# Kernel tuning notes

Measured on AMD Instinct MI355X. Metric: run time of the kernel, lower is better.

The kernel has to match this reference:

```python
import jax, jax.numpy as jnp
import numpy as np

DIM = 768
HEADS = 12
N_PATCH = 1024
ORDER = 5
DECAY = 0.5
EPS = 1e-6


def _exact_mask(N, order, decay):
    # 2D grid graph adjacency, row-major node order (matches sorted nx.grid_2d_graph nodes)
    side = int(np.sqrt(N))
    A = np.zeros((N, N), dtype=np.float64)
    idx = np.arange(N)
    r, c = idx // side, idx % side
    right = idx[c < side - 1]
    A[right, right + 1] = 1.0
    A[right + 1, right] = 1.0
    down = idx[r < side - 1]
    A[down, down + side] = 1.0
    A[down + side, down] = 1.0
    D_inv = 1.0 / np.maximum(A.sum(axis=1), 1.0)
    W = D_inv[:, None] * A
    M = np.eye(N)
    W_k = np.eye(N)
    coeff = 1.0
    for _ in range(order):
        W_k = W_k @ W
        coeff *= decay
        M += coeff * W_k
    M = M / M.sum(axis=1, keepdims=True)
    return jnp.asarray(M, dtype=jnp.float32)


def setup_inputs() -> dict:
    key = jax.random.key(0)
    k1, k2, k3, k4 = jax.random.split(key, 4)
    B = 4
    x = jax.random.normal(k1, (B, N_PATCH, DIM), dtype=jnp.float32)
    # nn.Linear(dim, 3*dim, bias=False): store as [dim, 3*dim] for x @ W
    scale = 1.0 / np.sqrt(DIM)
    W_qkv = jax.random.uniform(k2, (DIM, 3 * DIM), dtype=jnp.float32, minval=-scale, maxval=scale)
    W_out = jax.random.uniform(k3, (DIM, DIM), dtype=jnp.float32, minval=-scale, maxval=scale)
    b_out = jax.random.uniform(k4, (DIM,), dtype=jnp.float32, minval=-scale, maxval=scale)
    mask = _exact_mask(N_PATCH, ORDER, DECAY)
    return {"x": x, "W_qkv": W_qkv, "W_out": W_out, "b_out": b_out, "mask": mask}


def reference(x, W_qkv, W_out, b_out, mask):
    B, N, C = x.shape
    H, D = HEADS, C // HEADS
    qkv = x @ W_qkv  # [B, N, 3C]
    q, k, v = jnp.split(qkv, 3, axis=-1)
    # [B, N, C] -> [B, H, N, D]
    q, k, v = (t.reshape(B, N, H, D).transpose(0, 2, 1, 3) for t in (q, k, v))
    # feature map
    q = jax.nn.relu(q) + EPS
    k = jax.nn.relu(k) + EPS
    # (q^T @ M)^T = M^T @ q  ->  einsum over node axis
    q_graph = jnp.einsum('nm,bhnd->bhmd', mask, q)
    k_graph = jnp.einsum('nm,bhnd->bhmd', mask, k)
    q = q + 0.1 * q_graph
    k = k + 0.1 * k_graph
    linear_kernel = jnp.einsum('bhnd,bhmd->bhnm', q, k)  # [B, H, N, N]
    masked_kernel = linear_kernel * mask[None, None, :, :]
    z = 1.0 / (masked_kernel.sum(axis=-1, keepdims=True) + EPS)  # [B, H, N, 1]
    out = jnp.einsum('bhnm,bhmd->bhnd', masked_kernel, v) * z
    out = out.transpose(0, 2, 1, 3).reshape(B, N, C)
    return out @ W_out + b_out
```

## Files before the change

### kernel.cpp

```cpp
#include <hip/hip_runtime.h>

#define NP   1024
#define DIM  768
#define NH   12
#define HD   64
#define TQ   2304
#define EPS  1e-6f

typedef __attribute__((ext_vector_type(8))) short bf16x8;
typedef __attribute__((ext_vector_type(4))) float f32x4;

#define MFMA(a, b, c) __builtin_amdgcn_mfma_f32_16x16x32_bf16((a), (b), (c), 0, 0, 0)

__device__ __forceinline__ unsigned short f2b(float x) {
    unsigned int u = __builtin_bit_cast(unsigned int, x);
    u = (u + 0x7fffu + ((u >> 16) & 1u)) >> 16;
    return (unsigned short)u;
}
__device__ __forceinline__ float b2f(unsigned short h) {
    unsigned int u = ((unsigned int)h) << 16;
    return __builtin_bit_cast(float, u);
}
__device__ __forceinline__ void gld16(const void* g, void* l) {
    __builtin_amdgcn_global_load_lds((const __attribute__((address_space(1))) unsigned int*)g,
                                     (__attribute__((address_space(3))) unsigned int*)l,
                                     16, 0, 0);
}

__global__ __launch_bounds__(256) void k_prep(const float* __restrict__ x,
                                              const float* __restrict__ W_qkv,
                                              const float* __restrict__ W_out,
                                              const float* __restrict__ mask,
                                              unsigned short* __restrict__ xb,
                                              unsigned short* __restrict__ WqkvT,
                                              unsigned short* __restrict__ WoutT,
                                              unsigned short* __restrict__ maskT) {
    __shared__ float buf[64][65];
    const int bx = blockIdx.x, t = threadIdx.x;
    if (bx < 1536) {
        const int i = bx * 256 + t;
        const float4* p = (const float4*)x + (size_t)i * 2;
        float4 a = p[0], b = p[1];
        alignas(16) unsigned short o[8] = {f2b(a.x), f2b(a.y), f2b(a.z), f2b(a.w),
                                           f2b(b.x), f2b(b.y), f2b(b.z), f2b(b.w)};
        *(uint4*)(xb + (size_t)i * 8) = *(const uint4*)o;
        return;
    }
    const float* in; unsigned short* outp; int R, C, ct, rt;
    if (bx < 1968)      { int q = bx - 1536; in = W_qkv; outp = WqkvT; R = 768;  C = 2304; ct = q % 36; rt = q / 36; }
    else if (bx < 2112) { int q = bx - 1968; in = W_out; outp = WoutT; R = 768;  C = 768;  ct = q % 12; rt = q / 12; }
    else                { int q = bx - 2112; in = mask;  outp = maskT; R = 1024; C = 1024; ct = q % 16; rt = q / 16; }
    const int r0 = rt * 64, c0 = ct * 64;
    const int rr = t >> 4, cc = (t & 15) * 4;
    #pragma unroll
    for (int p = 0; p < 4; ++p) {
        float4 v = *(const float4*)(in + (size_t)(r0 + p * 16 + rr) * C + c0 + cc);
        buf[p * 16 + rr][cc + 0] = v.x; buf[p * 16 + rr][cc + 1] = v.y;
        buf[p * 16 + rr][cc + 2] = v.z; buf[p * 16 + rr][cc + 3] = v.w;
    }
    __syncthreads();
    const int oc = t >> 2, orr = (t & 3) * 16;
    alignas(16) unsigned short tmp[16];
    #pragma unroll
    for (int j = 0; j < 16; ++j) tmp[j] = f2b(buf[orr + j][oc]);
    unsigned short* dst = outp + (size_t)(c0 + oc) * R + r0 + orr;
    *(uint4*)dst = *(const uint4*)tmp;
    *(uint4*)(dst + 8) = *(const uint4*)(tmp + 8);
}

__global__ __launch_bounds__(256) void k_gemm1(const unsigned short* __restrict__ A,
                                               const unsigned short* __restrict__ Bt,
                                               unsigned short* __restrict__ T) {
    __shared__ unsigned short As[128][32];
    __shared__ unsigned short Bs[128][32];
    const int tid = threadIdx.x, w = tid >> 6, l = tid & 63;
    const int m0 = blockIdx.y * 128, n0 = blockIdx.x * 128;
    const int wm = (w >> 1) * 64, wn = (w & 1) * 64;
    const int quad = l >> 4, col = l & 15;
    const int lr = l >> 2, lc = (l & 3) * 8;

    f32x4 acc[4][4] = {};
    for (int k0 = 0; k0 < DIM; k0 += 32) {
        gld16(A + (size_t)(m0 + w * 32 + lr) * DIM + k0 + lc, &As[w * 32][0]);
        gld16(A + (size_t)(m0 + w * 32 + 16 + lr) * DIM + k0 + lc, &As[w * 32 + 16][0]);
        gld16(Bt + (size_t)(n0 + w * 32 + lr) * DIM + k0 + lc, &Bs[w * 32][0]);
        gld16(Bt + (size_t)(n0 + w * 32 + 16 + lr) * DIM + k0 + lc, &Bs[w * 32 + 16][0]);
        __syncthreads();
        bf16x8 a[4], b[4];
        #pragma unroll
        for (int i = 0; i < 4; ++i) a[i] = *(const bf16x8*)&As[wm + i * 16 + col][quad * 8];
        #pragma unroll
        for (int j = 0; j < 4; ++j) b[j] = *(const bf16x8*)&Bs[wn + j * 16 + col][quad * 8];
        #pragma unroll
        for (int i = 0; i < 4; ++i)
            #pragma unroll
            for (int j = 0; j < 4; ++j)
                acc[i][j] = MFMA(a[i], b[j], acc[i][j]);
        __syncthreads();
    }

    const int cgb = n0 + wn;
    const int slot = cgb / DIM;
    const int h = (cgb % DIM) >> 6;
    const bool act = (slot < 2);
    const int sh = slot * 48 + (m0 >> 10) * NH + h;
    const int npb = (m0 & 1023) + wm + quad * 4;
    #pragma unroll
    for (int j = 0; j < 4; ++j) {
        unsigned short* dcol = T + ((size_t)(sh * HD + j * 16 + col)) * NP + npb;
        #pragma unroll
        for (int i = 0; i < 4; ++i) {
            alignas(8) unsigned short t4[4];
            #pragma unroll
            for (int r = 0; r < 4; ++r) {
                float v = acc[i][j][r];
                if (act) v = fmaxf(v, 0.f) + EPS;
                t4[r] = f2b(v);
            }
            *(uint2*)(dcol + i * 16) = *(const uint2*)t4;
        }
    }
}

__global__ __launch_bounds__(256) void k_graphmix(const unsigned short* __restrict__ maskT,
                                                  const unsigned short* __restrict__ T,
                                                  unsigned short* __restrict__ q2) {
    const int bh = blockIdx.y, mt = blockIdx.x;
    const int m0 = mt * 64, gr = 2 * mt;
    __shared__ unsigned short Ms[64][32], Fq[64][32], Fk[64][32];
    __shared__ unsigned short Sq[64][72], Sk[64][72];
    const int tid = threadIdx.x, w = tid >> 6, l = tid & 63;
    const int quad = l >> 4, col = l & 15;
    const int lr = l >> 2, lc = (l & 3) * 8;
    const unsigned short* Tq = T + (size_t)bh * HD * NP;
    const unsigned short* Tk = T + (size_t)(48 + bh) * HD * NP;

    f32x4 accq[4] = {}, acck[4] = {};
    const int r0 = max(0, gr - 5), r1 = min(31, gr + 6);
    for (int rw = r0; rw <= r1; ++rw) {
        const int nc = rw * 32;
        __syncthreads();
        gld16(maskT + (size_t)(m0 + w * 16 + lr) * NP + nc + lc, &Ms[w * 16][0]);
        gld16(Tq + (size_t)(w * 16 + lr) * NP + nc + lc, &Fq[w * 16][0]);
        gld16(Tk + (size_t)(w * 16 + lr) * NP + nc + lc, &Fk[w * 16][0]);
        __syncthreads();
        if (rw == gr || rw == gr + 1) {
            const int off = (rw - gr) * 32;
            *(uint4*)&Sq[w * 16 + lr][off + lc] = *(const uint4*)&Fq[w * 16 + lr][lc];
            *(uint4*)&Sk[w * 16 + lr][off + lc] = *(const uint4*)&Fk[w * 16 + lr][lc];
        }
        bf16x8 a = *(const bf16x8*)&Ms[w * 16 + col][quad * 8];
        #pragma unroll
        for (int dt = 0; dt < 4; ++dt) {
            accq[dt] = MFMA(a, *(const bf16x8*)&Fq[dt * 16 + col][quad * 8], accq[dt]);
            acck[dt] = MFMA(a, *(const bf16x8*)&Fk[dt * 16 + col][quad * 8], acck[dt]);
        }
    }
    __syncthreads();
    unsigned short* q2q = q2 + ((size_t)bh * NP + m0) * HD;
    unsigned short* q2k = q2 + ((size_t)(48 + bh) * NP + m0) * HD;
    #pragma unroll
    for (int dt = 0; dt < 4; ++dt)
        #pragma unroll
        for (int r = 0; r < 4; ++r) {
            const int ml = w * 16 + quad * 4 + r;
            const int d = dt * 16 + col;
            q2q[(size_t)ml * HD + d] = f2b(b2f(Sq[d][ml]) + 0.1f * accq[dt][r]);
            q2k[(size_t)ml * HD + d] = f2b(b2f(Sk[d][ml]) + 0.1f * acck[dt][r]);
        }
}

__global__ __launch_bounds__(256) void k_attn(const unsigned short* __restrict__ q2,
                                              const unsigned short* __restrict__ T,
                                              const float* __restrict__ mask,
                                              unsigned short* __restrict__ attnb) {
    const int bh = blockIdx.y, b = bh / NH, h = bh % NH;
    const int nt2 = blockIdx.x, n0 = nt2 * 128;
    __shared__ unsigned short Qs[2][128][32];
    __shared__ unsigned short Ks[2][64][32];
    __shared__ unsigned short VT[2][64][32];
    __shared__ unsigned short Ss[128][72];
    __shared__ float rowz[128];
    const int tid = threadIdx.x, w = tid >> 6, l = tid & 63;
    const int quad = l >> 4, col = l & 15;
    const int lr = l >> 2, lc = (l & 3) * 8;

    const unsigned short* qb = q2 + ((size_t)bh * NP + n0) * HD;
    const unsigned short* kb = q2 + (size_t)(48 + bh) * NP * HD;
    const unsigned short* vtb = T + (size_t)(96 + bh) * HD * NP;

    #pragma unroll
    for (int hh = 0; hh < 2; ++hh)
        #pragma unroll
        for (int c = 0; c < 2; ++c)
            gld16(qb + (size_t)(w * 32 + c * 16 + lr) * HD + hh * 32 + lc,
                  &Qs[hh][w * 32 + c * 16][0]);

    f32x4 oacc[2][4] = {};
    float racc[2][4] = {};
    const int mlo = max(0, 2 * nt2 - 3), mhi = min(15, 2 * nt2 + 4);

    for (int mt = mlo; mt <= mhi; ++mt) {
        const int m0 = mt * 64;
        float mreg[2][4][4];
        #pragma unroll
        for (int rg = 0; rg < 2; ++rg)
            #pragma unroll
            for (int mtt = 0; mtt < 4; ++mtt)
                #pragma unroll
                for (int r = 0; r < 4; ++r)
                    mreg[rg][mtt][r] = mask[(size_t)(n0 + (w * 2 + rg) * 16 + quad * 4 + r) * NP
                                            + m0 + mtt * 16 + col];
        __syncthreads();
        #pragma unroll
        for (int hh = 0; hh < 2; ++hh) {
            gld16(kb + (size_t)(m0 + w * 16 + lr) * HD + hh * 32 + lc, &Ks[hh][w * 16][0]);
            gld16(vtb + (size_t)(w * 16 + lr) * NP + m0 + hh * 32 + lc, &VT[hh][w * 16][0]);
        }
        __syncthreads();

        f32x4 s[2][4] = {};
        #pragma unroll
        for (int ks = 0; ks < 2; ++ks) {
            bf16x8 bk[4];
            #pragma unroll
            for (int mtt = 0; mtt < 4; ++mtt) bk[mtt] = *(const bf16x8*)&Ks[ks][mtt * 16 + col][quad * 8];
            #pragma unroll
            for (int rg = 0; rg < 2; ++rg) {
                bf16x8 aq = *(const bf16x8*)&Qs[ks][(w * 2 + rg) * 16 + col][quad * 8];
                #pragma unroll
                for (int mtt = 0; mtt < 4; ++mtt) s[rg][mtt] = MFMA(aq, bk[mtt], s[rg][mtt]);
            }
        }
        #pragma unroll
        for (int rg = 0; rg < 2; ++rg)
            #pragma unroll
            for (int mtt = 0; mtt < 4; ++mtt)
                #pragma unroll
                for (int r = 0; r < 4; ++r) {
                    float v = s[rg][mtt][r] * mreg[rg][mtt][r];
                    racc[rg][r] += v;
                    Ss[(w * 2 + rg) * 16 + quad * 4 + r][mtt * 16 + col] = f2b(v);
                }
        __syncthreads();
        #pragma unroll
        for (int ks = 0; ks < 2; ++ks) {
            bf16x8 bv[4];
            #pragma unroll
            for (int dt = 0; dt < 4; ++dt) bv[dt] = *(const bf16x8*)&VT[ks][dt * 16 + col][quad * 8];
            #pragma unroll
            for (int rg = 0; rg < 2; ++rg) {
                bf16x8 as = *(const bf16x8*)&Ss[(w * 2 + rg) * 16 + col][ks * 32 + quad * 8];
                #pragma unroll
                for (int dt = 0; dt < 4; ++dt) oacc[rg][dt] = MFMA(as, bv[dt], oacc[rg][dt]);
            }
        }
    }

    #pragma unroll
    for (int rg = 0; rg < 2; ++rg)
        #pragma unroll
        for (int r = 0; r < 4; ++r) {
            float v = racc[rg][r];
            v += __shfl_xor(v, 1); v += __shfl_xor(v, 2);
            v += __shfl_xor(v, 4); v += __shfl_xor(v, 8);
            if (col == 0) rowz[(w * 2 + rg) * 16 + quad * 4 + r] = v;
        }
    __syncthreads();
    #pragma unroll
    for (int rg = 0; rg < 2; ++rg)
        #pragma unroll
        for (int r = 0; r < 4; ++r) {
            const int nl = (w * 2 + rg) * 16 + quad * 4 + r;
            const float z = 1.f / (rowz[nl] + EPS);
            #pragma unroll
            for (int dt = 0; dt < 4; ++dt)
                attnb[(size_t)(b * NP + n0 + nl) * DIM + h * HD + dt * 16 + col] =
                    f2b(oacc[rg][dt][r] * z);
        }
}

__global__ __launch_bounds__(256) void k_gemm2(const unsigned short* __restrict__ A,
                                               const unsigned short* __restrict__ Bt,
                                               const float* __restrict__ bias,
                                               float* __restrict__ C) {
    __shared__ unsigned short As[64][32];
    __shared__ unsigned short Bs[64][32];
    const int tid = threadIdx.x, w = tid >> 6, l = tid & 63;
    const int m0 = blockIdx.y * 64, n0 = blockIdx.x * 64;
    const int wm = (w >> 1) * 32, wn = (w & 1) * 32;
    const int quad = l >> 4, col = l & 15;
    const int lr = l >> 2, lc = (l & 3) * 8;

    f32x4 acc[2][2] = {};
    for (int k0 = 0; k0 < DIM; k0 += 32) {
        gld16(A + (size_t)(m0 + w * 16 + lr) * DIM + k0 + lc, &As[w * 16][0]);
        gld16(Bt + (size_t)(n0 + w * 16 + lr) * DIM + k0 + lc, &Bs[w * 16][0]);
        __syncthreads();
        bf16x8 a[2], b[2];
        #pragma unroll
        for (int i = 0; i < 2; ++i) a[i] = *(const bf16x8*)&As[wm + i * 16 + col][quad * 8];
        #pragma unroll
        for (int j = 0; j < 2; ++j) b[j] = *(const bf16x8*)&Bs[wn + j * 16 + col][quad * 8];
        #pragma unroll
        for (int i = 0; i < 2; ++i)
            #pragma unroll
            for (int j = 0; j < 2; ++j)
                acc[i][j] = MFMA(a[i], b[j], acc[i][j]);
        __syncthreads();
    }
    #pragma unroll
    for (int i = 0; i < 2; ++i)
        #pragma unroll
        for (int j = 0; j < 2; ++j) {
            const int n = n0 + wn + j * 16 + col;
            #pragma unroll
            for (int r = 0; r < 4; ++r) {
                const int m = m0 + wm + i * 16 + quad * 4 + r;
                C[(size_t)m * DIM + n] = acc[i][j][r] + bias[n];
            }
        }
}

extern "C" void kernel_launch(void* const* d_in, const int* in_sizes, int n_in,
                              void* d_out, int out_size, void* d_ws, size_t ws_size,
                              hipStream_t stream) {
    (void)in_sizes; (void)n_in; (void)out_size; (void)ws_size;
    const float* x     = (const float*)d_in[0];
    const float* W_qkv = (const float*)d_in[1];
    const float* W_out = (const float*)d_in[2];
    const float* b_out = (const float*)d_in[3];
    const float* mask  = (const float*)d_in[4];
    float* out = (float*)d_out;

    unsigned short* p = (unsigned short*)d_ws;
    unsigned short* xb    = p; p += (size_t)4096 * DIM;
    unsigned short* WqkvT = p; p += (size_t)TQ * DIM;
    unsigned short* WoutT = p; p += (size_t)DIM * DIM;
    unsigned short* maskT = p; p += (size_t)NP * NP;
    unsigned short* T     = p; p += (size_t)3 * 48 * HD * NP;
    unsigned short* q2    = p; p += (size_t)2 * 48 * NP * HD;
    unsigned short* attnb = p; p += (size_t)4096 * DIM;

    k_prep<<<dim3(2368), 256, 0, stream>>>(x, W_qkv, W_out, mask, xb, WqkvT, WoutT, maskT);
    k_gemm1<<<dim3(TQ / 128, 4096 / 128), 256, 0, stream>>>(xb, WqkvT, T);
    k_graphmix<<<dim3(NP / 64, 48), 256, 0, stream>>>(maskT, T, q2);
    k_attn<<<dim3(NP / 128, 48), 256, 0, stream>>>(q2, T, mask, attnb);
    k_gemm2<<<dim3(DIM / 64, 4096 / 64), 256, 0, stream>>>(attnb, WoutT, b_out, out);
}
```

Before: 175.4 us.

## Fold identity into graph mask, pack bf16 conversions, enlarge gemm2 tile

The prep kernel now builds M2 = I + 0.1*M^T once, so graphmix becomes a single banded matmul with no separate self-term staging. Graphmix walks 64-wide column chunks with double-width LDS tiles and writes its output as packed vectors. The attention score tile is stored as packed bf16 pairs and rebuilt with byte permutes. gemm1, graphmix and attention use a hardware packed bf16 convert, and gemm2 moves to 128x64 tiles. The aim is fewer instructions, less LDS traffic and fewer blocks, at the cost of rounding the identity term into bf16 and a changed band width for the mask.

```diff
diff --git a/kernel.cpp b/kernel.cpp
--- a/kernel.cpp
+++ b/kernel.cpp
@@ -21,6 +21,17 @@
     unsigned int u = ((unsigned int)h) << 16;
     return __builtin_bit_cast(float, u);
 }
+#if __has_builtin(__builtin_amdgcn_cvt_pk_bf16_f32)
+typedef __attribute__((ext_vector_type(2))) __bf16 bf16x2t;
+__device__ __forceinline__ unsigned int pk2(float lo, float hi) {
+    bf16x2t v = __builtin_amdgcn_cvt_pk_bf16_f32(lo, hi);
+    return __builtin_bit_cast(unsigned int, v);
+}
+#else
+__device__ __forceinline__ unsigned int pk2(float lo, float hi) {
+    return (unsigned int)f2b(lo) | ((unsigned int)f2b(hi) << 16);
+}
+#endif
 __device__ __forceinline__ void gld16(const void* g, void* l) {
     __builtin_amdgcn_global_load_lds((const __attribute__((address_space(1))) unsigned int*)g,
                                      (__attribute__((address_space(3))) unsigned int*)l,
@@ -34,7 +45,7 @@
                                               unsigned short* __restrict__ xb,
                                               unsigned short* __restrict__ WqkvT,
                                               unsigned short* __restrict__ WoutT,
-                                              unsigned short* __restrict__ maskT) {
+                                              unsigned short* __restrict__ M2) {
     __shared__ float buf[64][65];
     const int bx = blockIdx.x, t = threadIdx.x;
     if (bx < 1536) {
@@ -46,10 +57,10 @@
         *(uint4*)(xb + (size_t)i * 8) = *(const uint4*)o;
         return;
     }
-    const float* in; unsigned short* outp; int R, C, ct, rt;
+    const float* in; unsigned short* outp; int R, C, ct, rt; bool isMask = false;
     if (bx < 1968)      { int q = bx - 1536; in = W_qkv; outp = WqkvT; R = 768;  C = 2304; ct = q % 36; rt = q / 36; }
     else if (bx < 2112) { int q = bx - 1968; in = W_out; outp = WoutT; R = 768;  C = 768;  ct = q % 12; rt = q / 12; }
-    else                { int q = bx - 2112; in = mask;  outp = maskT; R = 1024; C = 1024; ct = q % 16; rt = q / 16; }
+    else                { int q = bx - 2112; in = mask;  outp = M2;    R = 1024; C = 1024; ct = q % 16; rt = q / 16; isMask = true; }
     const int r0 = rt * 64, c0 = ct * 64;
     const int rr = t >> 4, cc = (t & 15) * 4;
     #pragma unroll
@@ -61,8 +72,16 @@
     __syncthreads();
     const int oc = t >> 2, orr = (t & 3) * 16;
     alignas(16) unsigned short tmp[16];
-    #pragma unroll
-    for (int j = 0; j < 16; ++j) tmp[j] = f2b(buf[orr + j][oc]);
+    if (isMask) {
+        #pragma unroll
+        for (int j = 0; j < 16; ++j) {
+            float v = 0.1f * buf[orr + j][oc] + ((c0 + oc) == (r0 + orr + j) ? 1.f : 0.f);
+            tmp[j] = f2b(v);
+        }
+    } else {
+        #pragma unroll
+        for (int j = 0; j < 16; ++j) tmp[j] = f2b(buf[orr + j][oc]);
+    }
     unsigned short* dst = outp + (size_t)(c0 + oc) * R + r0 + orr;
     *(uint4*)dst = *(const uint4*)tmp;
     *(uint4*)(dst + 8) = *(const uint4*)(tmp + 8);
@@ -110,25 +129,23 @@
         unsigned short* dcol = T + ((size_t)(sh * HD + j * 16 + col)) * NP + npb;
         #pragma unroll
         for (int i = 0; i < 4; ++i) {
-            alignas(8) unsigned short t4[4];
-            #pragma unroll
-            for (int r = 0; r < 4; ++r) {
-                float v = acc[i][j][r];
-                if (act) v = fmaxf(v, 0.f) + EPS;
-                t4[r] = f2b(v);
-            }
-            *(uint2*)(dcol + i * 16) = *(const uint2*)t4;
-        }
-    }
-}
-
-__global__ __launch_bounds__(256) void k_graphmix(const unsigned short* __restrict__ maskT,
+            float v0 = acc[i][j][0], v1 = acc[i][j][1], v2 = acc[i][j][2], v3 = acc[i][j][3];
+            if (act) {
+                v0 = fmaxf(v0, 0.f) + EPS; v1 = fmaxf(v1, 0.f) + EPS;
+                v2 = fmaxf(v2, 0.f) + EPS; v3 = fmaxf(v3, 0.f) + EPS;
+            }
+            uint2 o; o.x = pk2(v0, v1); o.y = pk2(v2, v3);
+            *(uint2*)(dcol + i * 16) = o;
+        }
+    }
+}
+
+__global__ __launch_bounds__(256) void k_graphmix(const unsigned short* __restrict__ M2,
                                                   const unsigned short* __restrict__ T,
                                                   unsigned short* __restrict__ q2) {
     const int bh = blockIdx.y, mt = blockIdx.x;
-    const int m0 = mt * 64, gr = 2 * mt;
-    __shared__ unsigned short Ms[64][32], Fq[64][32], Fk[64][32];
-    __shared__ unsigned short Sq[64][72], Sk[64][72];
+    const int m0 = mt * 64;
+    __shared__ unsigned short M2s[2][64][32], Fq[2][64][32], Fk[2][64][32];
     const int tid = threadIdx.x, w = tid >> 6, l = tid & 63;
     const int quad = l >> 4, col = l & 15;
     const int lr = l >> 2, lc = (l & 3) * 8;
@@ -136,38 +153,39 @@
     const unsigned short* Tk = T + (size_t)(48 + bh) * HD * NP;
 
     f32x4 accq[4] = {}, acck[4] = {};
-    const int r0 = max(0, gr - 5), r1 = min(31, gr + 6);
-    for (int rw = r0; rw <= r1; ++rw) {
-        const int nc = rw * 32;
-        __syncthreads();
-        gld16(maskT + (size_t)(m0 + w * 16 + lr) * NP + nc + lc, &Ms[w * 16][0]);
-        gld16(Tq + (size_t)(w * 16 + lr) * NP + nc + lc, &Fq[w * 16][0]);
-        gld16(Tk + (size_t)(w * 16 + lr) * NP + nc + lc, &Fk[w * 16][0]);
-        __syncthreads();
-        if (rw == gr || rw == gr + 1) {
-            const int off = (rw - gr) * 32;
-            *(uint4*)&Sq[w * 16 + lr][off + lc] = *(const uint4*)&Fq[w * 16 + lr][lc];
-            *(uint4*)&Sk[w * 16 + lr][off + lc] = *(const uint4*)&Fk[w * 16 + lr][lc];
-        }
-        bf16x8 a = *(const bf16x8*)&Ms[w * 16 + col][quad * 8];
-        #pragma unroll
-        for (int dt = 0; dt < 4; ++dt) {
-            accq[dt] = MFMA(a, *(const bf16x8*)&Fq[dt * 16 + col][quad * 8], accq[dt]);
-            acck[dt] = MFMA(a, *(const bf16x8*)&Fk[dt * 16 + col][quad * 8], acck[dt]);
-        }
-    }
-    __syncthreads();
-    unsigned short* q2q = q2 + ((size_t)bh * NP + m0) * HD;
-    unsigned short* q2k = q2 + ((size_t)(48 + bh) * NP + m0) * HD;
-    #pragma unroll
-    for (int dt = 0; dt < 4; ++dt)
-        #pragma unroll
-        for (int r = 0; r < 4; ++r) {
-            const int ml = w * 16 + quad * 4 + r;
-            const int d = dt * 16 + col;
-            q2q[(size_t)ml * HD + d] = f2b(b2f(Sq[d][ml]) + 0.1f * accq[dt][r]);
-            q2k[(size_t)ml * HD + d] = f2b(b2f(Sk[d][ml]) + 0.1f * acck[dt][r]);
-        }
+    const int c0 = max(0, mt - 3), c1 = min(15, mt + 3);
+    for (int c = c0; c <= c1; ++c) {
+        const int nc = c * 64;
+        __syncthreads();
+        #pragma unroll
+        for (int hh = 0; hh < 2; ++hh) {
+            gld16(M2 + (size_t)(m0 + w * 16 + lr) * NP + nc + hh * 32 + lc, &M2s[hh][w * 16][0]);
+            gld16(Tq + (size_t)(w * 16 + lr) * NP + nc + hh * 32 + lc, &Fq[hh][w * 16][0]);
+            gld16(Tk + (size_t)(w * 16 + lr) * NP + nc + hh * 32 + lc, &Fk[hh][w * 16][0]);
+        }
+        __syncthreads();
+        #pragma unroll
+        for (int ks = 0; ks < 2; ++ks) {
+            bf16x8 bm = *(const bf16x8*)&M2s[ks][w * 16 + col][quad * 8];
+            #pragma unroll
+            for (int dt = 0; dt < 4; ++dt) {
+                bf16x8 aq = *(const bf16x8*)&Fq[ks][dt * 16 + col][quad * 8];
+                bf16x8 ak = *(const bf16x8*)&Fk[ks][dt * 16 + col][quad * 8];
+                accq[dt] = MFMA(aq, bm, accq[dt]);
+                acck[dt] = MFMA(ak, bm, acck[dt]);
+            }
+        }
+    }
+    unsigned short* q2q = q2 + ((size_t)bh * NP + m0 + w * 16 + col) * HD;
+    unsigned short* q2k = q2 + ((size_t)(48 + bh) * NP + m0 + w * 16 + col) * HD;
+    #pragma unroll
+    for (int dt = 0; dt < 4; ++dt) {
+        const int d0 = dt * 16 + quad * 4;
+        uint2 oq; oq.x = pk2(accq[dt][0], accq[dt][1]); oq.y = pk2(accq[dt][2], accq[dt][3]);
+        uint2 ok; ok.x = pk2(acck[dt][0], acck[dt][1]); ok.y = pk2(acck[dt][2], acck[dt][3]);
+        *(uint2*)(q2q + d0) = oq;
+        *(uint2*)(q2k + d0) = ok;
+    }
 }
 
 __global__ __launch_bounds__(256) void k_attn(const unsigned short* __restrict__ q2,
@@ -179,7 +197,7 @@
     __shared__ unsigned short Qs[2][128][32];
     __shared__ unsigned short Ks[2][64][32];
     __shared__ unsigned short VT[2][64][32];
-    __shared__ unsigned short Ss[128][72];
+    __shared__ unsigned int Ss2[64][68];
     __shared__ float rowz[128];
     const int tid = threadIdx.x, w = tid >> 6, l = tid & 63;
     const int quad = l >> 4, col = l & 15;
@@ -199,6 +217,7 @@
     f32x4 oacc[2][4] = {};
     float racc[2][4] = {};
     const int mlo = max(0, 2 * nt2 - 3), mhi = min(15, 2 * nt2 + 4);
+    const unsigned int sel = (col & 1) ? 0x07060302u : 0x05040100u;
 
     for (int mt = mlo; mt <= mhi; ++mt) {
         const int m0 = mt * 64;
@@ -233,15 +252,20 @@
             }
         }
         #pragma unroll
-        for (int rg = 0; rg < 2; ++rg)
-            #pragma unroll
-            for (int mtt = 0; mtt < 4; ++mtt)
-                #pragma unroll
-                for (int r = 0; r < 4; ++r) {
-                    float v = s[rg][mtt][r] * mreg[rg][mtt][r];
-                    racc[rg][r] += v;
-                    Ss[(w * 2 + rg) * 16 + quad * 4 + r][mtt * 16 + col] = f2b(v);
-                }
+        for (int rg = 0; rg < 2; ++rg) {
+            const int npr = (w * 2 + rg) * 8 + quad * 2;
+            #pragma unroll
+            for (int mtt = 0; mtt < 4; ++mtt) {
+                float v0 = s[rg][mtt][0] * mreg[rg][mtt][0];
+                float v1 = s[rg][mtt][1] * mreg[rg][mtt][1];
+                float v2 = s[rg][mtt][2] * mreg[rg][mtt][2];
+                float v3 = s[rg][mtt][3] * mreg[rg][mtt][3];
+                racc[rg][0] += v0; racc[rg][1] += v1;
+                racc[rg][2] += v2; racc[rg][3] += v3;
+                Ss2[npr][mtt * 16 + col]     = pk2(v0, v1);
+                Ss2[npr + 1][mtt * 16 + col] = pk2(v2, v3);
+            }
+        }
         __syncthreads();
         #pragma unroll
         for (int ks = 0; ks < 2; ++ks) {
@@ -250,7 +274,15 @@
             for (int dt = 0; dt < 4; ++dt) bv[dt] = *(const bf16x8*)&VT[ks][dt * 16 + col][quad * 8];
             #pragma unroll
             for (int rg = 0; rg < 2; ++rg) {
-                bf16x8 as = *(const bf16x8*)&Ss[(w * 2 + rg) * 16 + col][ks * 32 + quad * 8];
+                const unsigned int* rp = &Ss2[(w * 2 + rg) * 8 + (col >> 1)][ks * 32 + quad * 8];
+                uint4 U  = *(const uint4*)rp;
+                uint4 U2 = *(const uint4*)(rp + 4);
+                uint4 fr;
+                fr.x = __builtin_amdgcn_perm(U.y,  U.x,  sel);
+                fr.y = __builtin_amdgcn_perm(U.w,  U.z,  sel);
+                fr.z = __builtin_amdgcn_perm(U2.y, U2.x, sel);
+                fr.w = __builtin_amdgcn_perm(U2.w, U2.z, sel);
+                bf16x8 as = __builtin_bit_cast(bf16x8, fr);
                 #pragma unroll
                 for (int dt = 0; dt < 4; ++dt) oacc[rg][dt] = MFMA(as, bv[dt], oacc[rg][dt]);
             }
@@ -284,33 +316,34 @@
                                                const unsigned short* __restrict__ Bt,
                                                const float* __restrict__ bias,
                                                float* __restrict__ C) {
-    __shared__ unsigned short As[64][32];
+    __shared__ unsigned short As[128][32];
     __shared__ unsigned short Bs[64][32];
     const int tid = threadIdx.x, w = tid >> 6, l = tid & 63;
-    const int m0 = blockIdx.y * 64, n0 = blockIdx.x * 64;
-    const int wm = (w >> 1) * 32, wn = (w & 1) * 32;
+    const int m0 = blockIdx.y * 128, n0 = blockIdx.x * 64;
+    const int wm = (w >> 1) * 64, wn = (w & 1) * 32;
     const int quad = l >> 4, col = l & 15;
     const int lr = l >> 2, lc = (l & 3) * 8;
 
-    f32x4 acc[2][2] = {};
+    f32x4 acc[4][2] = {};
     for (int k0 = 0; k0 < DIM; k0 += 32) {
-        gld16(A + (size_t)(m0 + w * 16 + lr) * DIM + k0 + lc, &As[w * 16][0]);
+        gld16(A + (size_t)(m0 + w * 32 + lr) * DIM + k0 + lc, &As[w * 32][0]);
+        gld16(A + (size_t)(m0 + w * 32 + 16 + lr) * DIM + k0 + lc, &As[w * 32 + 16][0]);
         gld16(Bt + (size_t)(n0 + w * 16 + lr) * DIM + k0 + lc, &Bs[w * 16][0]);
         __syncthreads();
-        bf16x8 a[2], b[2];
-        #pragma unroll
-        for (int i = 0; i < 2; ++i) a[i] = *(const bf16x8*)&As[wm + i * 16 + col][quad * 8];
+        bf16x8 a[4], b[2];
+        #pragma unroll
+        for (int i = 0; i < 4; ++i) a[i] = *(const bf16x8*)&As[wm + i * 16 + col][quad * 8];
         #pragma unroll
         for (int j = 0; j < 2; ++j) b[j] = *(const bf16x8*)&Bs[wn + j * 16 + col][quad * 8];
         #pragma unroll
-        for (int i = 0; i < 2; ++i)
+        for (int i = 0; i < 4; ++i)
             #pragma unroll
             for (int j = 0; j < 2; ++j)
                 acc[i][j] = MFMA(a[i], b[j], acc[i][j]);
         __syncthreads();
     }
     #pragma unroll
-    for (int i = 0; i < 2; ++i)
+    for (int i = 0; i < 4; ++i)
         #pragma unroll
         for (int j = 0; j < 2; ++j) {
             const int n = n0 + wn + j * 16 + col;
@@ -337,14 +370,14 @@
     unsigned short* xb    = p; p += (size_t)4096 * DIM;
     unsigned short* WqkvT = p; p += (size_t)TQ * DIM;
     unsigned short* WoutT = p; p += (size_t)DIM * DIM;
-    unsigned short* maskT = p; p += (size_t)NP * NP;
+    unsigned short* M2    = p; p += (size_t)NP * NP;
     unsigned short* T     = p; p += (size_t)3 * 48 * HD * NP;
     unsigned short* q2    = p; p += (size_t)2 * 48 * NP * HD;
     unsigned short* attnb = p; p += (size_t)4096 * DIM;
 
-    k_prep<<<dim3(2368), 256, 0, stream>>>(x, W_qkv, W_out, mask, xb, WqkvT, WoutT, maskT);
+    k_prep<<<dim3(2368), 256, 0, stream>>>(x, W_qkv, W_out, mask, xb, WqkvT, WoutT, M2);
     k_gemm1<<<dim3(TQ / 128, 4096 / 128), 256, 0, stream>>>(xb, WqkvT, T);
-    k_graphmix<<<dim3(NP / 64, 48), 256, 0, stream>>>(maskT, T, q2);
+    k_graphmix<<<dim3(NP / 64, 48), 256, 0, stream>>>(M2, T, q2);
     k_attn<<<dim3(NP / 128, 48), 256, 0, stream>>>(q2, T, mask, attnb);
-    k_gemm2<<<dim3(DIM / 64, 4096 / 64), 256, 0, stream>>>(attnb, WoutT, b_out, out);
-}
+    k_gemm2<<<dim3(DIM / 64, 4096 / 128), 256, 0, stream>>>(attnb, WoutT, b_out, out);
+}
```

Measured after the change: 176.2 us. About the same (+0.5%).
